# Kernel tuning notes

Measured on AMD Instinct MI355X. Metric: run time of the kernel, lower is better.

## Reference

```python
import jax, jax.numpy as jnp
import numpy as np

N_NODES = 100000
N_EDGES = 3200000
D_IN = 256
D_HID = 256


def spmm(edge_row, edge_col, edge_val, h):
    # neigh[i] = sum_{e: row[e]==i} val[e] * h[col[e]]   (COO sparse @ dense)
    msgs = edge_val[:, None] * h[edge_col]          # [E, D]
    return jax.ops.segment_sum(msgs, edge_row, num_segments=N_NODES)


def setup_inputs() -> dict:
    key = jax.random.key(0)
    ks = jax.random.split(key, 8)
    x = jax.random.normal(ks[0], (N_NODES, D_IN), dtype=jnp.float32)
    edge_row = jax.random.randint(ks[1], (N_EDGES,), 0, N_NODES, dtype=jnp.int32)
    edge_col = jax.random.randint(ks[2], (N_EDGES,), 0, N_NODES, dtype=jnp.int32)
    edge_val = jax.random.uniform(ks[3], (N_EDGES,), dtype=jnp.float32) / 32.0  # ~mean-normalized
    W1 = jax.random.normal(ks[4], (2 * D_IN, D_HID), dtype=jnp.float32) * (1.0 / np.sqrt(2 * D_IN))
    b1 = jnp.zeros((D_HID,), dtype=jnp.float32)
    Wout = jax.random.normal(ks[5], (2 * D_HID, D_HID), dtype=jnp.float32) * (1.0 / np.sqrt(2 * D_HID))
    bout = jnp.zeros((D_HID,), dtype=jnp.float32)
    return {"x": x, "edge_row": edge_row, "edge_col": edge_col, "edge_val": edge_val,
            "W1": W1, "b1": b1, "Wout": Wout, "bout": bout}


def reference(x, edge_row, edge_col, edge_val, W1, b1, Wout, bout):
    # Layer 1: SpMM aggregate -> concat -> linear -> relu  (dropout inactive: eval mode)
    h = x
    neigh = spmm(edge_row, edge_col, edge_val, h)
    h = jnp.concatenate([h, neigh], axis=1)          # [N, 2*D]
    h = jax.nn.relu(h @ W1 + b1)
    # Output layer: SpMM aggregate -> concat -> linear (no activation)
    neigh = spmm(edge_row, edge_col, edge_val, h)
    h = jnp.concatenate([h, neigh], axis=1)
    z = h @ Wout + bout
    return z
```

## Files before the change

kernel.cpp:

```cpp
#include <hip/hip_runtime.h>
#include <cstddef>
#include <cstdint>

#define N_NODES 100000
#define N_EDGES 3200000
#define D 256
#define BSHIFT 9
#define NBUCK ((N_NODES + (1 << BSHIFT) - 1) >> BSHIFT)
#define EPB 4096
#define CAP 20480

typedef __attribute__((ext_vector_type(8))) short bf16x8;
typedef __attribute__((ext_vector_type(4))) float f32x4;
typedef __attribute__((ext_vector_type(2))) float f32x2;
typedef unsigned int u32;

#if defined(__has_builtin)
#if __has_builtin(__builtin_amdgcn_cvt_pk_f32_fp8) && __has_builtin(__builtin_amdgcn_cvt_pk_fp8_f32)
#define FP8_BUILTINS 1
#endif
#endif
#ifndef FP8_BUILTINS
#include <hip/hip_fp8.h>
#endif

__device__ __forceinline__ void fp8x4_to_f32(u32 d, float* f) {
#ifdef FP8_BUILTINS
    f32x2 lo = __builtin_amdgcn_cvt_pk_f32_fp8(d, false);
    f32x2 hi = __builtin_amdgcn_cvt_pk_f32_fp8(d, true);
    f[0] = lo.x; f[1] = lo.y; f[2] = hi.x; f[3] = hi.y;
#else
    __hip_fp8_e4m3 t;
#pragma unroll
    for (int i = 0; i < 4; ++i) { t.__x = (unsigned char)((d >> (8 * i)) & 0xff); f[i] = (float)t; }
#endif
}

__device__ __forceinline__ u32 f32x4_to_fp8(float a, float b, float c, float d) {
#ifdef FP8_BUILTINS
    u32 q = __builtin_amdgcn_cvt_pk_fp8_f32(a, b, 0u, false);
    return __builtin_amdgcn_cvt_pk_fp8_f32(c, d, q, true);
#else
    return (u32)__hip_fp8_e4m3(a).__x | ((u32)__hip_fp8_e4m3(b).__x << 8) |
           ((u32)__hip_fp8_e4m3(c).__x << 16) | ((u32)__hip_fp8_e4m3(d).__x << 24);
#endif
}

#define GLOAD16(gsrc, ldst)                                                      \
    __builtin_amdgcn_global_load_lds(                                            \
        (const __attribute__((address_space(1))) void*)(gsrc),                   \
        (__attribute__((address_space(3))) void*)(ldst), 16, 0, 0)

__device__ __forceinline__ ushort f2b(float f) {
    unsigned u = __float_as_uint(f);
    return (ushort)((u + 0x7fffu + ((u >> 16) & 1u)) >> 16);
}

__global__ __launch_bounds__(256) void binpass1_kernel(const int* __restrict__ erow,
                                                       const int* __restrict__ ecol,
                                                       const float* __restrict__ evalv,
                                                       int* __restrict__ bucket_cursor,
                                                       int2* __restrict__ staging) {
    __shared__ int cnt[NBUCK];
    __shared__ int lstart[NBUCK];
    __shared__ int gbase[NBUCK];
    __shared__ int wtot[4];
    __shared__ int woff[4];
    __shared__ int2 lcv[EPB];
    __shared__ unsigned char lbb[EPB];
    const int tid = threadIdx.x;
    const size_t base = (size_t)blockIdx.x * EPB;
    for (int b = tid; b < NBUCK; b += 256) cnt[b] = 0;
    __syncthreads();
    int bb[16];
    int2 pcv[16];
    int loff[16];
#pragma unroll
    for (int i = 0; i < 16; ++i) {
        size_t e = base + (size_t)i * 256 + tid;
        if (e < N_EDGES) {
            int r = erow[e];
            int b = r >> BSHIFT;
            bb[i] = b;
            pcv[i] = make_int2(ecol[e] | ((r & ((1 << BSHIFT) - 1)) << 17),
                               __float_as_int(evalv[e]));
            loff[i] = atomicAdd(&cnt[b], 1);
        } else {
            bb[i] = -1;
        }
    }
    __syncthreads();
    {
        int b = tid;
        int v = (b < NBUCK) ? cnt[b] : 0;
        int lane = tid & 63, wv = tid >> 6;
        int inc = v;
#pragma unroll
        for (int off = 1; off < 64; off <<= 1) {
            int u = __shfl_up(inc, off, 64);
            if (lane >= off) inc += u;
        }
        if (lane == 63) wtot[wv] = inc;
        __syncthreads();
        if (tid == 0) {
            int run = 0;
#pragma unroll
            for (int w = 0; w < 4; ++w) { woff[w] = run; run += wtot[w]; }
        }
        __syncthreads();
        int exc = woff[wv] + inc - v;
        if (b < NBUCK) {
            lstart[b] = exc;
            if (v > 0) gbase[b] = atomicAdd(&bucket_cursor[b], v);
        }
    }
    __syncthreads();
#pragma unroll
    for (int i = 0; i < 16; ++i) {
        if (bb[i] >= 0) {
            int p = lstart[bb[i]] + loff[i];
            lcv[p] = pcv[i];
            lbb[p] = (unsigned char)bb[i];
        }
    }
    __syncthreads();
    const int total = lstart[NBUCK - 1] + cnt[NBUCK - 1];
    for (int p = tid; p < total; p += 256) {
        int b = lbb[p];
        int g = gbase[b] + (p - lstart[b]);
        staging[g] = lcv[p];
    }
}

__global__ __launch_bounds__(256) void binpass2_kernel(const int* __restrict__ bucket_cursor,
                                                       const int2* __restrict__ staging,
                                                       int2* __restrict__ cedge,
                                                       int2* __restrict__ rowrange) {
    __shared__ int cnt[1 << BSHIFT];
    __shared__ int scur[1 << BSHIFT];
    __shared__ int wtot[4];
    __shared__ int woff[4];
    const int b   = blockIdx.x;
    const int tid = threadIdx.x;
    const int base = b * CAP;
    const int hi   = bucket_cursor[b];
    for (int i = tid; i < (1 << BSHIFT); i += 256) cnt[i] = 0;
    __syncthreads();
    for (int k = base + tid; k < hi; k += 256)
        atomicAdd(&cnt[((u32)staging[k].x) >> 17], 1);
    __syncthreads();
    int v0 = cnt[2 * tid];
    int v1 = cnt[2 * tid + 1];
    int s = v0 + v1;
    int lane = tid & 63, wv = tid >> 6;
    int inc = s;
#pragma unroll
    for (int off = 1; off < 64; off <<= 1) {
        int u = __shfl_up(inc, off, 64);
        if (lane >= off) inc += u;
    }
    if (lane == 63) wtot[wv] = inc;
    __syncthreads();
    if (tid == 0) {
        int run = 0;
#pragma unroll
        for (int w = 0; w < 4; ++w) { woff[w] = run; run += wtot[w]; }
    }
    __syncthreads();
    int exc = woff[wv] + inc - s;
    int g0 = base + exc;
    scur[2 * tid]     = g0;
    scur[2 * tid + 1] = g0 + v0;
    const int r0 = b << BSHIFT;
    int r = r0 + 2 * tid;
    if (r < N_NODES)     rowrange[r]     = make_int2(g0, g0 + v0);
    if (r + 1 < N_NODES) rowrange[r + 1] = make_int2(g0 + v0, g0 + v0 + v1);
    __syncthreads();
    for (int k = base + tid; k < hi; k += 256) {
        int2 e = staging[k];
        int rloc = ((u32)e.x) >> 17;
        int pos = atomicAdd(&scur[rloc], 1);
        cedge[pos] = make_int2(e.x & 0x1FFFF, e.y);
    }
}

__global__ __launch_bounds__(256) void cvt_kernel(const float* __restrict__ in,
                                                  ushort* __restrict__ out, int n4,
                                                  int* __restrict__ bucket_cursor,
                                                  u32* __restrict__ outq) {
    int i = blockIdx.x * 256 + threadIdx.x;
    if (blockIdx.x == 0 && threadIdx.x < NBUCK)
        bucket_cursor[threadIdx.x] = threadIdx.x * CAP;
    if (i < n4) {
        float4 v = ((const float4*)in)[i];
        uint2 p;
        p.x = (unsigned)f2b(v.x) | ((unsigned)f2b(v.y) << 16);
        p.y = (unsigned)f2b(v.z) | ((unsigned)f2b(v.w) << 16);
        ((uint2*)out)[i] = p;
        outq[i] = f32x4_to_fp8(v.x, v.y, v.z, v.w);
    }
}

__global__ __launch_bounds__(256) void wtrans_kernel(const float* __restrict__ W1,
                                                     const float* __restrict__ Wout,
                                                     ushort* __restrict__ W1sz,
                                                     ushort* __restrict__ Woutsz) {
    int t = blockIdx.x * 256 + threadIdx.x;
    const float* W = (t < 131072) ? W1 : Wout;
    ushort* Wsz    = (t < 131072) ? W1sz : Woutsz;
    int u = t & 131071;
    int j = u & 255;
    int k = u >> 8;
    int dst = j * 512 + ((((k >> 3) ^ (j & 63)) << 3) | (k & 7));
    Wsz[dst] = f2b(W[(size_t)k * 256 + j]);
}

__global__ __launch_bounds__(256) void spmm_kernel(const int2* __restrict__ rowrange,
                                                   const int2* __restrict__ cedge,
                                                   const unsigned char* __restrict__ hq,
                                                   ushort* __restrict__ outb) {
    const int node = (blockIdx.x << 2) + (threadIdx.x >> 6);
    const int lane = threadIdx.x & 63;
    const u32* __restrict__ h1 = (const u32*)hq + lane;
    int2 rr = rowrange[node];
    int k = rr.x;
    const int end = rr.y;
    float a0 = 0.f, a1 = 0.f, a2 = 0.f, a3 = 0.f;
#define EDGE_FMA(e, d)                                              \
    {                                                               \
        float v = __int_as_float((e).y);                            \
        float f[4];                                                 \
        fp8x4_to_f32((d), f);                                       \
        a0 = fmaf(v, f[0], a0); a1 = fmaf(v, f[1], a1);             \
        a2 = fmaf(v, f[2], a2); a3 = fmaf(v, f[3], a3);             \
    }
    for (; k + 8 <= end; k += 8) {
        int2 e[8];
#pragma unroll
        for (int i = 0; i < 8; ++i) e[i] = cedge[k + i];
        u32 d[8];
#pragma unroll
        for (int i = 0; i < 8; ++i) d[i] = h1[(u32)e[i].x * 64];
#pragma unroll
        for (int i = 0; i < 8; ++i) EDGE_FMA(e[i], d[i])
    }
    for (; k < end; ++k) {
        int2 e = cedge[k];
        u32 d = h1[(u32)e.x * 64];
        EDGE_FMA(e, d)
    }
#undef EDGE_FMA
    uint2 p;
    p.x = (unsigned)f2b(a0) | ((unsigned)f2b(a1) << 16);
    p.y = (unsigned)f2b(a2) | ((unsigned)f2b(a3) << 16);
    ((uint2*)outb)[(size_t)node * 64 + lane] = p;
}

template <bool OUT_BF16>
__global__ __launch_bounds__(512, 2) void gemm_mfma_kernel(const ushort* __restrict__ A1,
                                                           const ushort* __restrict__ A2,
                                                           const ushort* __restrict__ Wsz,
                                                           const float* __restrict__ bias,
                                                           void* __restrict__ outp,
                                                           unsigned char* __restrict__ outq) {
    __shared__ __align__(16) char lds[163840];
    const int tid  = threadIdx.x;
    const int wid  = tid >> 6;
    const int lane = tid & 63;
    const int lr   = lane & 15;
    const int g    = lane >> 4;
    const int bm   = blockIdx.x * 128;
    const int c0   = blockIdx.y * 128;
    char* const ldsA = lds + 131072 + wid * 4096;

    int arow = bm + wid * 16 + (lane >> 2);
    if (arow >= N_NODES) arow = N_NODES - 1;
    const int acol = (lane & 3) * 8;

#define STAGE_A(tt)                                                              \
    {                                                                            \
        const ushort* As_ = ((tt) < 8) ? A1 : A2;                                \
        GLOAD16(As_ + (size_t)arow * 256 + ((tt) & 7) * 32 + acol,               \
                ldsA + ((tt) & 3) * 1024);                                       \
    }

    int jbyte[8], jx[8];
#pragma unroll
    for (int cf = 0; cf < 8; ++cf) {
        int jl = cf * 16 + lr;
        jbyte[cf] = jl * 1024;
        jx[cf] = jl & 63;
    }

#pragma unroll
    for (int q = 0; q < 16; ++q)
        GLOAD16(Wsz + (size_t)c0 * 512 + (wid * 16 + q) * 512 + lane * 8,
                lds + (wid * 16 + q) * 1024);
    STAGE_A(0)
    STAGE_A(1)
    STAGE_A(2)
    asm volatile("s_waitcnt vmcnt(2)" ::: "memory");
    __builtin_amdgcn_sched_barrier(0);
    __builtin_amdgcn_s_barrier();

    f32x4 acc[8];
#pragma unroll
    for (int cf = 0; cf < 8; ++cf) acc[cf] = (f32x4){0.f, 0.f, 0.f, 0.f};

#pragma unroll 1
    for (int t = 0; t < 16; ++t) {
        if (t < 13) {
            STAGE_A(t + 3)
            asm volatile("s_waitcnt vmcnt(3)" ::: "memory");
        } else if (t == 13) {
            asm volatile("s_waitcnt vmcnt(2)" ::: "memory");
        } else if (t == 14) {
            asm volatile("s_waitcnt vmcnt(1)" ::: "memory");
        } else {
            asm volatile("s_waitcnt vmcnt(0)" ::: "memory");
        }
        __builtin_amdgcn_sched_barrier(0);
        const char* Ab = ldsA + (t & 3) * 1024;
        bf16x8 af = *(const bf16x8*)(Ab + lr * 64 + g * 16);
        const int cbase = t * 4 + g;
#pragma unroll
        for (int cf = 0; cf < 8; ++cf) {
            bf16x8 bf_ = *(const bf16x8*)(lds + jbyte[cf] + ((cbase ^ jx[cf]) << 4));
            acc[cf] = __builtin_amdgcn_mfma_f32_16x16x32_bf16(af, bf_, acc[cf], 0, 0, 0);
        }
    }
#undef STAGE_A

    float bv[8];
#pragma unroll
    for (int cf = 0; cf < 8; ++cf) bv[cf] = bias[c0 + cf * 16 + lr];

    if (!OUT_BF16) {
        float* out = (float*)outp;
#pragma unroll
        for (int reg = 0; reg < 4; ++reg) {
            int row = bm + wid * 16 + g * 4 + reg;
            if (row < N_NODES) {
#pragma unroll
                for (int cf = 0; cf < 8; ++cf)
                    out[(size_t)row * 256 + c0 + cf * 16 + lr] = acc[cf][reg] + bv[cf];
            }
        }
    } else {
        __builtin_amdgcn_s_barrier();
        ushort* out = (ushort*)outp;
        float (*L)[132] = (float(*)[132])(lds + wid * 16384);
#pragma unroll
        for (int cf = 0; cf < 8; ++cf)
#pragma unroll
            for (int reg = 0; reg < 4; ++reg)
                L[g * 4 + reg][cf * 16 + lr] = fmaxf(acc[cf][reg] + bv[cf], 0.f);
        asm volatile("s_waitcnt lgkmcnt(0)" ::: "memory");
        __builtin_amdgcn_sched_barrier(0);
        const int r  = lane >> 2;
        const int cq = lane & 3;
        const int grow = bm + wid * 16 + r;
        if (grow < N_NODES) {
#pragma unroll
            for (int q = 0; q < 4; ++q) {
                int col = q * 32 + cq * 8;
                float4 u0 = *(const float4*)&L[r][col];
                float4 u1 = *(const float4*)&L[r][col + 4];
                uint4 w4;
                w4.x = (unsigned)f2b(u0.x) | ((unsigned)f2b(u0.y) << 16);
                w4.y = (unsigned)f2b(u0.z) | ((unsigned)f2b(u0.w) << 16);
                w4.z = (unsigned)f2b(u1.x) | ((unsigned)f2b(u1.y) << 16);
                w4.w = (unsigned)f2b(u1.z) | ((unsigned)f2b(u1.w) << 16);
                *(uint4*)&out[(size_t)grow * 256 + c0 + col] = w4;
                uint2 q8;
                q8.x = f32x4_to_fp8(u0.x, u0.y, u0.z, u0.w);
                q8.y = f32x4_to_fp8(u1.x, u1.y, u1.z, u1.w);
                *(uint2*)&outq[(size_t)grow * 256 + c0 + col] = q8;
            }
        }
    }
}

extern "C" void kernel_launch(void* const* d_in, const int* in_sizes, int n_in,
                              void* d_out, int out_size, void* d_ws, size_t ws_size,
                              hipStream_t stream) {
    const float* x     = (const float*)d_in[0];
    const int*   erow  = (const int*)d_in[1];
    const int*   ecol  = (const int*)d_in[2];
    const float* evalv = (const float*)d_in[3];
    const float* W1    = (const float*)d_in[4];
    const float* b1    = (const float*)d_in[5];
    const float* Wout  = (const float*)d_in[6];
    const float* bout  = (const float*)d_in[7];
    float* out = (float*)d_out;

    char* ws = (char*)d_ws;
    size_t off = 0;
    auto alloc = [&](size_t bytes) -> void* {
        void* p = ws + off;
        off += (bytes + 255) & ~(size_t)255;
        return p;
    };
    ushort* xb       = (ushort*)alloc((size_t)N_NODES * D * 2);
    ushort* h1b      = (ushort*)alloc((size_t)N_NODES * D * 2);
    ushort* neighb   = (ushort*)alloc((size_t)N_NODES * D * 2);
    unsigned char* xq  = (unsigned char*)alloc((size_t)N_NODES * D);
    unsigned char* h1q = (unsigned char*)alloc((size_t)N_NODES * D);
    ushort* W1sz     = (ushort*)alloc((size_t)512 * 256 * 2);
    ushort* Woutsz   = (ushort*)alloc((size_t)512 * 256 * 2);
    int*    bcursor  = (int*)alloc((size_t)NBUCK * sizeof(int));
    int2*   rowrange = (int2*)alloc((size_t)N_NODES * sizeof(int2));
    int2*   staging  = (int2*)alloc((size_t)NBUCK * CAP * sizeof(int2));
    int2*   cedge    = (int2*)alloc((size_t)NBUCK * CAP * sizeof(int2));

    cvt_kernel<<<(N_NODES * D / 4 + 255) / 256, 256, 0, stream>>>(x, xb, N_NODES * D / 4,
                                                                  bcursor, (u32*)xq);
    wtrans_kernel<<<1024, 256, 0, stream>>>(W1, Wout, W1sz, Woutsz);

    binpass1_kernel<<<(N_EDGES + EPB - 1) / EPB, 256, 0, stream>>>(erow, ecol, evalv,
                                                                   bcursor, staging);
    binpass2_kernel<<<NBUCK, 256, 0, stream>>>(bcursor, staging, cedge, rowrange);

    dim3 ggrid((N_NODES + 127) / 128, 2);
    const int sgrid = N_NODES / 4;
    spmm_kernel<<<sgrid, 256, 0, stream>>>(rowrange, cedge, xq, neighb);
    gemm_mfma_kernel<true><<<ggrid, 512, 0, stream>>>(xb, neighb, W1sz, b1, h1b, h1q);
    spmm_kernel<<<sgrid, 256, 0, stream>>>(rowrange, cedge, h1q, neighb);
    gemm_mfma_kernel<false><<<ggrid, 512, 0, stream>>>(h1b, neighb, Woutsz, bout, out, nullptr);
}
```

Measured before the change: 479.1 us.

## Make GEMM persistent so each block loads weights once and loops over row tiles

The GEMM kernel becomes persistent: 512 blocks, each fixed to one 128-column half, loop over row tiles with stride 256. The weight slice and bias are loaded into LDS once per block instead of once per tile. The bf16/fp8 epilogue now goes through the per-wave A staging buffer in two 8-row halves, so it no longer overwrites the weight region. Launch bounds drop to one block per CU, and the weight-prefetch overlap with the first A stages is gone, which may leave latency exposed at the start of each tile.

```diff
diff --git a/kernel.cpp b/kernel.cpp
--- a/kernel.cpp
+++ b/kernel.cpp
@@ -9,6 +9,7 @@
 #define NBUCK ((N_NODES + (1 << BSHIFT) - 1) >> BSHIFT)
 #define EPB 4096
 #define CAP 20480
+#define NTILE ((N_NODES + 127) / 128)
 
 typedef __attribute__((ext_vector_type(8))) short bf16x8;
 typedef __attribute__((ext_vector_type(4))) float f32x4;
@@ -257,7 +258,7 @@
 }
 
 template <bool OUT_BF16>
-__global__ __launch_bounds__(512, 2) void gemm_mfma_kernel(const ushort* __restrict__ A1,
+__global__ __launch_bounds__(512, 1) void gemm_mfma_kernel(const ushort* __restrict__ A1,
                                                            const ushort* __restrict__ A2,
                                                            const ushort* __restrict__ Wsz,
                                                            const float* __restrict__ bias,
@@ -269,14 +270,30 @@
     const int lane = tid & 63;
     const int lr   = lane & 15;
     const int g    = lane >> 4;
-    const int bm   = blockIdx.x * 128;
-    const int c0   = blockIdx.y * 128;
+    const int c0     = (blockIdx.x & 1) * 128;
+    const int pairId = blockIdx.x >> 1;
     char* const ldsA = lds + 131072 + wid * 4096;
-
-    int arow = bm + wid * 16 + (lane >> 2);
-    if (arow >= N_NODES) arow = N_NODES - 1;
     const int acol = (lane & 3) * 8;
 
+#pragma unroll
+    for (int q = 0; q < 16; ++q)
+        GLOAD16(Wsz + (size_t)c0 * 512 + (wid * 16 + q) * 512 + lane * 8,
+                lds + (wid * 16 + q) * 1024);
+    float bv[8];
+#pragma unroll
+    for (int cf = 0; cf < 8; ++cf) bv[cf] = bias[c0 + cf * 16 + lr];
+    int jbyte[8], jx[8];
+#pragma unroll
+    for (int cf = 0; cf < 8; ++cf) {
+        int jl = cf * 16 + lr;
+        jbyte[cf] = jl * 1024;
+        jx[cf] = jl & 63;
+    }
+    asm volatile("s_waitcnt vmcnt(0)" ::: "memory");
+    __builtin_amdgcn_sched_barrier(0);
+    __builtin_amdgcn_s_barrier();
+
+    int arow;
 #define STAGE_A(tt)                                                              \
     {                                                                            \
         const ushort* As_ = ((tt) < 8) ? A1 : A2;                                \
@@ -284,101 +301,100 @@
                 ldsA + ((tt) & 3) * 1024);                                       \
     }
 
-    int jbyte[8], jx[8];
-#pragma unroll
-    for (int cf = 0; cf < 8; ++cf) {
-        int jl = cf * 16 + lr;
-        jbyte[cf] = jl * 1024;
-        jx[cf] = jl & 63;
-    }
-
-#pragma unroll
-    for (int q = 0; q < 16; ++q)
-        GLOAD16(Wsz + (size_t)c0 * 512 + (wid * 16 + q) * 512 + lane * 8,
-                lds + (wid * 16 + q) * 1024);
-    STAGE_A(0)
-    STAGE_A(1)
-    STAGE_A(2)
-    asm volatile("s_waitcnt vmcnt(2)" ::: "memory");
-    __builtin_amdgcn_sched_barrier(0);
-    __builtin_amdgcn_s_barrier();
-
-    f32x4 acc[8];
-#pragma unroll
-    for (int cf = 0; cf < 8; ++cf) acc[cf] = (f32x4){0.f, 0.f, 0.f, 0.f};
-
 #pragma unroll 1
-    for (int t = 0; t < 16; ++t) {
-        if (t < 13) {
-            STAGE_A(t + 3)
-            asm volatile("s_waitcnt vmcnt(3)" ::: "memory");
-        } else if (t == 13) {
-            asm volatile("s_waitcnt vmcnt(2)" ::: "memory");
-        } else if (t == 14) {
-            asm volatile("s_waitcnt vmcnt(1)" ::: "memory");
+    for (int tile = pairId; tile < NTILE; tile += 256) {
+        const int bm = tile * 128;
+        arow = bm + wid * 16 + (lane >> 2);
+        if (arow >= N_NODES) arow = N_NODES - 1;
+        STAGE_A(0)
+        STAGE_A(1)
+        STAGE_A(2)
+
+        f32x4 acc[8];
+#pragma unroll
+        for (int cf = 0; cf < 8; ++cf) acc[cf] = (f32x4){0.f, 0.f, 0.f, 0.f};
+
+#pragma unroll 1
+        for (int t = 0; t < 16; ++t) {
+            if (t < 13) {
+                STAGE_A(t + 3)
+                asm volatile("s_waitcnt vmcnt(3)" ::: "memory");
+            } else if (t == 13) {
+                asm volatile("s_waitcnt vmcnt(2)" ::: "memory");
+            } else if (t == 14) {
+                asm volatile("s_waitcnt vmcnt(1)" ::: "memory");
+            } else {
+                asm volatile("s_waitcnt vmcnt(0)" ::: "memory");
+            }
+            __builtin_amdgcn_sched_barrier(0);
+            const char* Ab = ldsA + (t & 3) * 1024;
+            bf16x8 af = *(const bf16x8*)(Ab + lr * 64 + g * 16);
+            const int cbase = t * 4 + g;
+#pragma unroll
+            for (int cf = 0; cf < 8; ++cf) {
+                bf16x8 bf_ = *(const bf16x8*)(lds + jbyte[cf] + ((cbase ^ jx[cf]) << 4));
+                acc[cf] = __builtin_amdgcn_mfma_f32_16x16x32_bf16(af, bf_, acc[cf], 0, 0, 0);
+            }
+        }
+
+        if (!OUT_BF16) {
+            float* out = (float*)outp;
+#pragma unroll
+            for (int reg = 0; reg < 4; ++reg) {
+                int row = bm + wid * 16 + g * 4 + reg;
+                if (row < N_NODES) {
+#pragma unroll
+                    for (int cf = 0; cf < 8; ++cf)
+                        out[(size_t)row * 256 + c0 + cf * 16 + lr] = acc[cf][reg] + bv[cf];
+                }
+            }
         } else {
-            asm volatile("s_waitcnt vmcnt(0)" ::: "memory");
-        }
-        __builtin_amdgcn_sched_barrier(0);
-        const char* Ab = ldsA + (t & 3) * 1024;
-        bf16x8 af = *(const bf16x8*)(Ab + lr * 64 + g * 16);
-        const int cbase = t * 4 + g;
-#pragma unroll
-        for (int cf = 0; cf < 8; ++cf) {
-            bf16x8 bf_ = *(const bf16x8*)(lds + jbyte[cf] + ((cbase ^ jx[cf]) << 4));
-            acc[cf] = __builtin_amdgcn_mfma_f32_16x16x32_bf16(af, bf_, acc[cf], 0, 0, 0);
+            ushort* out = (ushort*)outp;
+            float (*L8)[128] = (float(*)[128])ldsA;
+#pragma unroll 1
+            for (int half = 0; half < 2; ++half) {
+                if ((g >> 1) == half) {
+#pragma unroll
+                    for (int cf = 0; cf < 8; ++cf)
+#pragma unroll
+                        for (int reg = 0; reg < 4; ++reg)
+                            L8[(g & 1) * 4 + reg][cf * 16 + lr] =
+                                fmaxf(acc[cf][reg] + bv[cf], 0.f);
+                }
+                asm volatile("s_waitcnt lgkmcnt(0)" ::: "memory");
+                __builtin_amdgcn_sched_barrier(0);
+                const int row8 = lane >> 3;
+                const int cb = (lane & 7) * 16;
+                const int grow = bm + wid * 16 + half * 8 + row8;
+                if (grow < N_NODES) {
+                    float4 u0 = *(const float4*)&L8[row8][cb];
+                    float4 u1 = *(const float4*)&L8[row8][cb + 4];
+                    float4 u2 = *(const float4*)&L8[row8][cb + 8];
+                    float4 u3 = *(const float4*)&L8[row8][cb + 12];
+                    uint4 w0, w1;
+                    w0.x = (unsigned)f2b(u0.x) | ((unsigned)f2b(u0.y) << 16);
+                    w0.y = (unsigned)f2b(u0.z) | ((unsigned)f2b(u0.w) << 16);
+                    w0.z = (unsigned)f2b(u1.x) | ((unsigned)f2b(u1.y) << 16);
+                    w0.w = (unsigned)f2b(u1.z) | ((unsigned)f2b(u1.w) << 16);
+                    w1.x = (unsigned)f2b(u2.x) | ((unsigned)f2b(u2.y) << 16);
+                    w1.y = (unsigned)f2b(u2.z) | ((unsigned)f2b(u2.w) << 16);
+                    w1.z = (unsigned)f2b(u3.x) | ((unsigned)f2b(u3.y) << 16);
+                    w1.w = (unsigned)f2b(u3.z) | ((unsigned)f2b(u3.w) << 16);
+                    *(uint4*)&out[(size_t)grow * 256 + c0 + cb]     = w0;
+                    *(uint4*)&out[(size_t)grow * 256 + c0 + cb + 8] = w1;
+                    uint4 q8;
+                    q8.x = f32x4_to_fp8(u0.x, u0.y, u0.z, u0.w);
+                    q8.y = f32x4_to_fp8(u1.x, u1.y, u1.z, u1.w);
+                    q8.z = f32x4_to_fp8(u2.x, u2.y, u2.z, u2.w);
+                    q8.w = f32x4_to_fp8(u3.x, u3.y, u3.z, u3.w);
+                    *(uint4*)&outq[(size_t)grow * 256 + c0 + cb] = q8;
+                }
+                asm volatile("s_waitcnt lgkmcnt(0)" ::: "memory");
+                __builtin_amdgcn_sched_barrier(0);
+            }
         }
     }
 #undef STAGE_A
-
-    float bv[8];
-#pragma unroll
-    for (int cf = 0; cf < 8; ++cf) bv[cf] = bias[c0 + cf * 16 + lr];
-
-    if (!OUT_BF16) {
-        float* out = (float*)outp;
-#pragma unroll
-        for (int reg = 0; reg < 4; ++reg) {
-            int row = bm + wid * 16 + g * 4 + reg;
-            if (row < N_NODES) {
-#pragma unroll
-                for (int cf = 0; cf < 8; ++cf)
-                    out[(size_t)row * 256 + c0 + cf * 16 + lr] = acc[cf][reg] + bv[cf];
-            }
-        }
-    } else {
-        __builtin_amdgcn_s_barrier();
-        ushort* out = (ushort*)outp;
-        float (*L)[132] = (float(*)[132])(lds + wid * 16384);
-#pragma unroll
-        for (int cf = 0; cf < 8; ++cf)
-#pragma unroll
-            for (int reg = 0; reg < 4; ++reg)
-                L[g * 4 + reg][cf * 16 + lr] = fmaxf(acc[cf][reg] + bv[cf], 0.f);
-        asm volatile("s_waitcnt lgkmcnt(0)" ::: "memory");
-        __builtin_amdgcn_sched_barrier(0);
-        const int r  = lane >> 2;
-        const int cq = lane & 3;
-        const int grow = bm + wid * 16 + r;
-        if (grow < N_NODES) {
-#pragma unroll
-            for (int q = 0; q < 4; ++q) {
-                int col = q * 32 + cq * 8;
-                float4 u0 = *(const float4*)&L[r][col];
-                float4 u1 = *(const float4*)&L[r][col + 4];
-                uint4 w4;
-                w4.x = (unsigned)f2b(u0.x) | ((unsigned)f2b(u0.y) << 16);
-                w4.y = (unsigned)f2b(u0.z) | ((unsigned)f2b(u0.w) << 16);
-                w4.z = (unsigned)f2b(u1.x) | ((unsigned)f2b(u1.y) << 16);
-                w4.w = (unsigned)f2b(u1.z) | ((unsigned)f2b(u1.w) << 16);
-                *(uint4*)&out[(size_t)grow * 256 + c0 + col] = w4;
-                uint2 q8;
-                q8.x = f32x4_to_fp8(u0.x, u0.y, u0.z, u0.w);
-                q8.y = f32x4_to_fp8(u1.x, u1.y, u1.z, u1.w);
-                *(uint2*)&outq[(size_t)grow * 256 + c0 + col] = q8;
-            }
-        }
-    }
 }
 
 extern "C" void kernel_launch(void* const* d_in, const int* in_sizes, int n_in,
@@ -421,10 +437,9 @@
                                                                    bcursor, staging);
     binpass2_kernel<<<NBUCK, 256, 0, stream>>>(bcursor, staging, cedge, rowrange);
 
-    dim3 ggrid((N_NODES + 127) / 128, 2);
     const int sgrid = N_NODES / 4;
     spmm_kernel<<<sgrid, 256, 0, stream>>>(rowrange, cedge, xq, neighb);
-    gemm_mfma_kernel<true><<<ggrid, 512, 0, stream>>>(xb, neighb, W1sz, b1, h1b, h1q);
+    gemm_mfma_kernel<true><<<512, 512, 0, stream>>>(xb, neighb, W1sz, b1, h1b, h1q);
     spmm_kernel<<<sgrid, 256, 0, stream>>>(rowrange, cedge, h1q, neighb);
-    gemm_mfma_kernel<false><<<ggrid, 512, 0, stream>>>(h1b, neighb, Woutsz, bout, out, nullptr);
-}
+    gemm_mfma_kernel<false><<<512, 512, 0, stream>>>(h1b, neighb, Woutsz, bout, out, nullptr);
+}
```

Result: faster. 467.3 us, median of 2 (-2.5%).
